# Kernel optimization log

Hardware: AMD Instinct MI355X
Metric: run time of the kernel (lower is better)

## Reference

```python
import jax, jax.numpy as jnp
import numpy as np

B, S, E, NUM_CLASSES = 4, 4096, 256, 16

def setup_inputs() -> dict:
    key = jax.random.key(0)
    ks = jax.random.split(key, 10)
    std = E ** -0.5
    return {
        "x":  jax.random.normal(ks[0], (B, S, E), dtype=jnp.float32),
        "wq": jax.random.normal(ks[1], (E, E), dtype=jnp.float32) * std,
        "bq": jnp.zeros((E,), dtype=jnp.float32),
        "wk": jax.random.normal(ks[2], (E, E), dtype=jnp.float32) * std,
        "bk": jnp.zeros((E,), dtype=jnp.float32),
        "wv": jax.random.normal(ks[3], (E, E), dtype=jnp.float32) * std,
        "bv": jnp.zeros((E,), dtype=jnp.float32),
        "wo": jax.random.normal(ks[4], (NUM_CLASSES, E), dtype=jnp.float32) * std,
        "bo": jnp.zeros((NUM_CLASSES,), dtype=jnp.float32),
    }

def reference(x, wq, bq, wk, bk, wv, bv, wo, bo):
    embed_dim = wq.shape[0]
    scaling = embed_dim ** -0.5  # float(embed_dim) ** (-0.5)
    # torch Linear: y = x @ W.T + b
    Q = jnp.einsum('bse,oe->bso', x, wq) + bq
    K = jnp.einsum('bse,oe->bso', x, wk) + bk
    V = jnp.einsum('bse,oe->bso', x, wv) + bv
    # scores: [B, S, S]
    scores = jnp.einsum('bqe,bke->bqk', Q, K) * scaling
    # original code has `/ (embed_dim ^ 0.5)`; intended math is / sqrt(embed_dim)
    attn = jax.nn.softmax(scores, axis=-1) * scaling
    attn_out = jnp.einsum('bqk,bke->bqe', attn, V)
    return jnp.einsum('bqe,oe->bqo', attn_out, wo) + bo
```

## Files before the change

kernel.cpp:

```cpp
#include <hip/hip_runtime.h>
#include <hip/hip_bf16.h>


#define S_ 4096
#define E_ 256
#define B_ 4
#define NC_ 16
#define BS_ (B_ * S_)
#define NS_ 4

typedef __attribute__((ext_vector_type(8))) short bf16x8;
typedef __attribute__((ext_vector_type(4))) float f32x4;

__device__ __forceinline__ unsigned short bf16_rtne(float f) {
    unsigned int u = __float_as_uint(f);
    return (unsigned short)((u + 0x7FFFu + ((u >> 16) & 1u)) >> 16);
}
__device__ __forceinline__ bf16x8 pack8(f32x4 a, f32x4 b) {
    bf16x8 r;
#pragma unroll
    for (int i = 0; i < 4; i++) r[i] = (short)bf16_rtne(a[i]);
#pragma unroll
    for (int i = 0; i < 4; i++) r[4 + i] = (short)bf16_rtne(b[i]);
    return r;
}
__device__ __forceinline__ void gl_lds16(const void* g, void* lds) {
    __builtin_amdgcn_global_load_lds(
        (const __attribute__((address_space(1))) unsigned int*)g,
        (__attribute__((address_space(3))) unsigned int*)lds, 16, 0, 0);
}

__global__ __launch_bounds__(256) void qkv_gemm(
    const float* __restrict__ x, const float* __restrict__ wq,
    const float* __restrict__ wk, const float* __restrict__ wv,
    const float* __restrict__ bq, const float* __restrict__ bk,
    const float* __restrict__ bv, short* __restrict__ Qb,
    short* __restrict__ Kb, short* __restrict__ Vtc) {
    __shared__ bf16x8 xt[256];
    __shared__ bf16x8 wt[1024];
    __shared__ short epi[16896];

    int t = threadIdx.x;
    int sel = blockIdx.x, m0 = blockIdx.y * 64;
    int lane = t & 63, wid = t >> 6, quad = lane >> 4, idx = lane & 15;

    const float* w = (sel == 0) ? wq : (sel == 1) ? wk : wv;
    const float* bias = (sel == 0) ? bq : (sel == 1) ? bk : bv;

    const float* xsrc = x + (size_t)(m0 + (t >> 2)) * E_ + (t & 3) * 8;

    f32x4 zf = {0.f, 0.f, 0.f, 0.f};
    f32x4 acc[16];
#pragma unroll
    for (int i = 0; i < 16; i++) acc[i] = zf;

    for (int kc = 0; kc < E_; kc += 32) {
        f32x4 a0 = *(const f32x4*)(xsrc + kc);
        f32x4 a1 = *(const f32x4*)(xsrc + kc + 4);
        xt[t] = pack8(a0, a1);
#pragma unroll
        for (int i = 0; i < 4; i++) {
            int p = i * 256 + t;
            const float* ws = w + (size_t)(p >> 2) * E_ + (p & 3) * 8 + kc;
            f32x4 b0 = *(const f32x4*)ws;
            f32x4 b1 = *(const f32x4*)(ws + 4);
            wt[p] = pack8(b0, b1);
        }
        __syncthreads();
        bf16x8 af = xt[(wid * 16 + idx) * 4 + quad];
#pragma unroll
        for (int ct = 0; ct < 16; ct++)
            acc[ct] = __builtin_amdgcn_mfma_f32_16x16x32_bf16(
                af, wt[(ct * 16 + idx) * 4 + quad], acc[ct], 0, 0, 0);
        __syncthreads();
    }

    int qr = quad * 4;
    if (sel == 2) {
#pragma unroll
        for (int ct = 0; ct < 16; ct++) {
            int e = ct * 16 + idx;
            float bb = bias[e];
#pragma unroll
            for (int r = 0; r < 4; r++) {
                int mr = wid * 16 + qr + r;
                int ckg = mr >> 5, sin = mr & 31;
                int sp = ((sin & 15) << 1) | (sin >> 4);
                int pos = (sp >> 3) ^ ((e >> 1) & 3);
                epi[ckg * 8192 + e * 32 + pos * 8 + (sp & 7)] =
                    (short)bf16_rtne(acc[ct][r] + bb);
            }
        }
        __syncthreads();
        size_t base = ((size_t)((m0 >> 12) * 128 + ((m0 & (S_ - 1)) >> 5))) * 8192;
#pragma unroll
        for (int j = 0; j < 8; j++) {
            int unit = j * 256 + t;
            *(bf16x8*)(Vtc + base + (size_t)unit * 8) = *(const bf16x8*)&epi[unit * 8];
        }
    } else {
        float alpha = (sel == 0) ? 0.0625f : 1.0f;
#pragma unroll
        for (int ct = 0; ct < 16; ct++) {
            int n = ct * 16 + idx;
            float bb = bias[n];
#pragma unroll
            for (int r = 0; r < 4; r++) {
                int row = wid * 16 + qr + r;
                int col = (sel == 1) ? ((((n >> 3) ^ (row & 7)) << 3) | (n & 7)) : n;
                epi[row * 264 + col] = (short)bf16_rtne((acc[ct][r] + bb) * alpha);
            }
        }
        __syncthreads();
        short* out = (sel == 0) ? Qb : Kb;
#pragma unroll
        for (int j = 0; j < 8; j++) {
            int g = j * 256 + t;
            int row = g >> 5, seg = g & 31;
            *(bf16x8*)(out + (size_t)(m0 + row) * E_ + seg * 8) =
                *(const bf16x8*)&epi[row * 264 + seg * 8];
        }
    }
}

__global__ __launch_bounds__(256, 2) void flash_attn(
    const short* __restrict__ Qb, const short* __restrict__ Kb,
    const short* __restrict__ Vtc, short* __restrict__ Opart,
    float* __restrict__ lpart) {
    __shared__ __align__(16) short lds[36864];

    int t = threadIdx.x;
    int b = blockIdx.z, slice = blockIdx.y, q0 = blockIdx.x * 128;
    int key0 = slice * (S_ / NS_);
    const int nchunk = (S_ / NS_) / 32;
    int lane = t & 63, wv = t >> 6, quad = lane >> 4, idx = lane & 15;

    bf16x8 qf[2][8];
#pragma unroll
    for (int u = 0; u < 2; u++) {
        const short* qrow = Qb + (size_t)(b * S_ + q0 + u * 64 + wv * 16 + idx) * E_ + quad * 8;
#pragma unroll
        for (int c = 0; c < 8; c++) qf[u][c] = *(const bf16x8*)(qrow + c * 32);
    }

    f32x4 zf = {0.f, 0.f, 0.f, 0.f};
    f32x4 oacc[2][16];
#pragma unroll
    for (int u = 0; u < 2; u++)
#pragma unroll
        for (int i = 0; i < 16; i++) oacc[u][i] = zf;
    float ls[2][4] = {{0, 0, 0, 0}, {0, 0, 0, 0}};

    const short* kg = Kb + (size_t)(b * S_ + key0) * E_ + lane * 8;
    const short* vg = Vtc + ((size_t)(b * 128 + (key0 >> 5))) * 8192 + lane * 8;
    short* psw = lds + 32768 + wv * 1024;
    unsigned int* pswu = (unsigned int*)psw;
    int vsw = (quad ^ ((idx >> 1) & 3)) << 3;

#pragma unroll
    for (int j = 0; j < 4; j++) gl_lds16(kg + (wv * 4 + j) * 512, &lds[(wv * 4 + j) * 512]);
#pragma unroll
    for (int j = 0; j < 4; j++) gl_lds16(vg + (wv * 4 + j) * 512, &lds[16384 + (wv * 4 + j) * 512]);
#pragma unroll
    for (int j = 0; j < 4; j++) gl_lds16(kg + 8192 + (wv * 4 + j) * 512, &lds[8192 + (wv * 4 + j) * 512]);
    __syncthreads();

    {
        f32x4 s[4] = {zf, zf, zf, zf};
#pragma unroll
        for (int c = 0; c < 8; c++) {
            int p = (((c * 4 + quad) ^ (idx & 7)) << 3);
            bf16x8 k0 = *(const bf16x8*)&lds[idx * 256 + p];
            bf16x8 k1 = *(const bf16x8*)&lds[(16 + idx) * 256 + p];
            s[0] = __builtin_amdgcn_mfma_f32_16x16x32_bf16(qf[0][c], k0, s[0], 0, 0, 0);
            s[1] = __builtin_amdgcn_mfma_f32_16x16x32_bf16(qf[0][c], k1, s[1], 0, 0, 0);
            s[2] = __builtin_amdgcn_mfma_f32_16x16x32_bf16(qf[1][c], k0, s[2], 0, 0, 0);
            s[3] = __builtin_amdgcn_mfma_f32_16x16x32_bf16(qf[1][c], k1, s[3], 0, 0, 0);
        }
#pragma unroll
        for (int u = 0; u < 2; u++)
#pragma unroll
            for (int r = 0; r < 4; r++) {
                float p0 = __expf(s[u * 2][r]);
                float p1 = __expf(s[u * 2 + 1][r]);
                ls[u][r] += p0 + p1;
                pswu[u * 256 + (quad * 4 + r) * 16 + idx] =
                    (unsigned int)bf16_rtne(p0) | ((unsigned int)bf16_rtne(p1) << 16);
            }
    }

    for (int ck = 0; ck < nchunk - 1; ck++) {
        __syncthreads();
        if (ck + 2 < nchunk) {
            const short* ks = kg + (size_t)(ck + 2) * 8192;
            short* kd = lds + (ck & 1) * 8192;
#pragma unroll
            for (int j = 0; j < 4; j++) gl_lds16(ks + (wv * 4 + j) * 512, &kd[(wv * 4 + j) * 512]);
        }
        {
            const short* vs = vg + (size_t)(ck + 1) * 8192;
            short* vd = lds + 16384 + ((ck + 1) & 1) * 8192;
#pragma unroll
            for (int j = 0; j < 4; j++) gl_lds16(vs + (wv * 4 + j) * 512, &vd[(wv * 4 + j) * 512]);
        }
        const short* kc = lds + ((ck + 1) & 1) * 8192;
        f32x4 s[4] = {zf, zf, zf, zf};
#pragma unroll
        for (int c = 0; c < 8; c++) {
            int p = (((c * 4 + quad) ^ (idx & 7)) << 3);
            bf16x8 k0 = *(const bf16x8*)&kc[idx * 256 + p];
            bf16x8 k1 = *(const bf16x8*)&kc[(16 + idx) * 256 + p];
            s[0] = __builtin_amdgcn_mfma_f32_16x16x32_bf16(qf[0][c], k0, s[0], 0, 0, 0);
            s[1] = __builtin_amdgcn_mfma_f32_16x16x32_bf16(qf[0][c], k1, s[1], 0, 0, 0);
            s[2] = __builtin_amdgcn_mfma_f32_16x16x32_bf16(qf[1][c], k0, s[2], 0, 0, 0);
            s[3] = __builtin_amdgcn_mfma_f32_16x16x32_bf16(qf[1][c], k1, s[3], 0, 0, 0);
        }
        bf16x8 af0 = *(const bf16x8*)&psw[idx * 32 + quad * 8];
        bf16x8 af1 = *(const bf16x8*)&psw[512 + idx * 32 + quad * 8];
#pragma unroll
        for (int u = 0; u < 2; u++)
#pragma unroll
            for (int r = 0; r < 4; r++) {
                float p0 = __expf(s[u * 2][r]);
                float p1 = __expf(s[u * 2 + 1][r]);
                ls[u][r] += p0 + p1;
                pswu[u * 256 + (quad * 4 + r) * 16 + idx] =
                    (unsigned int)bf16_rtne(p0) | ((unsigned int)bf16_rtne(p1) << 16);
            }
        const short* vc = lds + 16384 + (ck & 1) * 8192;
#pragma unroll
        for (int ct = 0; ct < 16; ct++) {
            bf16x8 v = *(const bf16x8*)&vc[(ct * 16 + idx) * 32 + vsw];
            oacc[0][ct] = __builtin_amdgcn_mfma_f32_16x16x32_bf16(af0, v, oacc[0][ct], 0, 0, 0);
            oacc[1][ct] = __builtin_amdgcn_mfma_f32_16x16x32_bf16(af1, v, oacc[1][ct], 0, 0, 0);
        }
    }
    __syncthreads();
    {
        bf16x8 af0 = *(const bf16x8*)&psw[idx * 32 + quad * 8];
        bf16x8 af1 = *(const bf16x8*)&psw[512 + idx * 32 + quad * 8];
        const short* vc = lds + 16384 + ((nchunk - 1) & 1) * 8192;
#pragma unroll
        for (int ct = 0; ct < 16; ct++) {
            bf16x8 v = *(const bf16x8*)&vc[(ct * 16 + idx) * 32 + vsw];
            oacc[0][ct] = __builtin_amdgcn_mfma_f32_16x16x32_bf16(af0, v, oacc[0][ct], 0, 0, 0);
            oacc[1][ct] = __builtin_amdgcn_mfma_f32_16x16x32_bf16(af1, v, oacc[1][ct], 0, 0, 0);
        }
    }
    __syncthreads();

#pragma unroll
    for (int u = 0; u < 2; u++)
#pragma unroll
        for (int r = 0; r < 4; r++) {
            float v = ls[u][r];
            v += __shfl_xor(v, 1);
            v += __shfl_xor(v, 2);
            v += __shfl_xor(v, 4);
            v += __shfl_xor(v, 8);
            if (idx == 0)
                lpart[(size_t)slice * BS_ + b * S_ + q0 + u * 64 + wv * 16 + quad * 4 + r] = v;
        }

    short* scr = lds + wv * 8192;
#pragma unroll
    for (int u = 0; u < 2; u++)
#pragma unroll
        for (int ct = 0; ct < 16; ct++) {
            int e = ct * 16 + idx;
#pragma unroll
            for (int r = 0; r < 4; r++) {
                int lr = quad * 4 + r;
                scr[u * 4096 + lr * 256 + ((((e >> 3) ^ (lr & 7)) << 3) | (e & 7))] =
                    (short)bf16_rtne(oacc[u][ct][r]);
            }
        }
#pragma unroll
    for (int u = 0; u < 2; u++) {
        size_t obase = ((size_t)slice * BS_ + (size_t)b * S_ + q0 + u * 64 + wv * 16) * E_;
#pragma unroll
        for (int j = 0; j < 8; j++) {
            int unit = j * 64 + lane;
            *(bf16x8*)(Opart + obase + (size_t)unit * 8) =
                *(const bf16x8*)&scr[u * 4096 + unit * 8];
        }
    }
}

__global__ __launch_bounds__(256) void proj_out(
    const short* __restrict__ Opart, const float* __restrict__ lpart,
    const float* __restrict__ wo, const float* __restrict__ bo,
    float* __restrict__ out) {
    __shared__ __align__(16) short at2[2][16384];
    int t = threadIdx.x;
    int m0 = blockIdx.x * 64;
    int lane = t & 63, wv = t >> 6, quad = lane >> 4, idx = lane & 15;

    bf16x8 bw[8];
#pragma unroll
    for (int c = 0; c < 8; c++) {
        const float* ws = wo + idx * E_ + c * 32 + quad * 8;
        f32x4 w0 = *(const f32x4*)ws;
        f32x4 w1 = *(const f32x4*)(ws + 4);
        bw[c] = pack8(w0, w1);
    }

#pragma unroll
    for (int j = 0; j < 8; j++)
        gl_lds16(Opart + (size_t)m0 * E_ + (wv * 8 + j) * 512 + lane * 8,
                 &at2[0][(wv * 8 + j) * 512]);

    f32x4 acc = {0.f, 0.f, 0.f, 0.f};
    for (int ns = 0; ns < NS_; ns++) {
        __syncthreads();
        if (ns + 1 < NS_) {
            const short* src = Opart + ((size_t)(ns + 1) * BS_ + m0) * E_ + lane * 8;
#pragma unroll
            for (int j = 0; j < 8; j++)
                gl_lds16(src + (wv * 8 + j) * 512, &at2[(ns + 1) & 1][(wv * 8 + j) * 512]);
        }
        const short* a = at2[ns & 1];
#pragma unroll
        for (int c = 0; c < 8; c++) {
            bf16x8 af = *(const bf16x8*)&a[(wv * 16 + idx) * 256 +
                                           ((((c * 4 + quad) ^ (idx & 7)) << 3))];
            acc = __builtin_amdgcn_mfma_f32_16x16x32_bf16(af, bw[c], acc, 0, 0, 0);
        }
    }
#pragma unroll
    for (int r = 0; r < 4; r++) {
        int m = m0 + wv * 16 + quad * 4 + r;
        float ltot = 0.f;
#pragma unroll
        for (int ns = 0; ns < NS_; ns++) ltot += lpart[(size_t)ns * BS_ + m];
        out[(size_t)m * NC_ + idx] = acc[r] * (0.0625f / ltot) + bo[idx];
    }
}

extern "C" void kernel_launch(void* const* d_in, const int* in_sizes, int n_in,
                              void* d_out, int out_size, void* d_ws, size_t ws_size,
                              hipStream_t stream) {
    const float* x  = (const float*)d_in[0];
    const float* wq = (const float*)d_in[1];
    const float* bq = (const float*)d_in[2];
    const float* wk = (const float*)d_in[3];
    const float* bk = (const float*)d_in[4];
    const float* wv = (const float*)d_in[5];
    const float* bv = (const float*)d_in[6];
    const float* wo = (const float*)d_in[7];
    const float* bo = (const float*)d_in[8];
    float* out = (float*)d_out;

    const size_t NEL = (size_t)BS_ * E_;
    short* Qb = (short*)d_ws;
    short* Kb = Qb + NEL;
    short* Vtc = Kb + NEL;
    short* Opart = Vtc + NEL;
    float* lpart = (float*)(Opart + (size_t)NS_ * NEL);

    qkv_gemm<<<dim3(3, BS_ / 64), 256, 0, stream>>>(x, wq, wk, wv, bq, bk, bv, Qb, Kb, Vtc);
    flash_attn<<<dim3(S_ / 128, NS_, B_), 256, 0, stream>>>(Qb, Kb, Vtc, Opart, lpart);
    proj_out<<<BS_ / 64, 256, 0, stream>>>(Opart, lpart, wo, bo, out);
}
```

Measured before the change: 178.9 us.

## Prepack x/W to bf16, double-buffer QKV GEMM loads, add MFMA priority and padding

Adds a pre-pass kernel that converts x and the three weight matrices to bf16 once, writing into the Opart workspace before it is used. The QKV GEMM then streams bf16 tiles into double-buffered swizzled LDS with direct global-to-LDS loads, removing the per-block fp32 conversion and one barrier per step. The attention kernel raises wave priority around MFMA blocks and pads the P scratch row stride to cut LDS bank conflicts. The cost is an extra launch and a full extra pass over x in memory.

```diff
diff --git a/kernel.cpp b/kernel.cpp
--- a/kernel.cpp
+++ b/kernel.cpp
@@ -29,50 +29,86 @@
         (const __attribute__((address_space(1))) unsigned int*)g,
         (__attribute__((address_space(3))) unsigned int*)lds, 16, 0, 0);
 }
-
-__global__ __launch_bounds__(256) void qkv_gemm(
+__device__ __forceinline__ int swz_u(int q) { return q ^ ((q >> 3) & 7); }
+
+#define XUNITS_ (BS_ * E_ / 8)
+#define WUNITS_ (3 * E_ * E_ / 8)
+__global__ __launch_bounds__(256) void pack_xw(
     const float* __restrict__ x, const float* __restrict__ wq,
     const float* __restrict__ wk, const float* __restrict__ wv,
+    short* __restrict__ xb, short* __restrict__ wb) {
+    int u = blockIdx.x * 256 + threadIdx.x;
+    const float* src;
+    short* dst;
+    if (u < XUNITS_) {
+        src = x + (size_t)u * 8;
+        dst = xb + (size_t)u * 8;
+    } else {
+        int u2 = u - XUNITS_;
+        int sel = u2 >> 13;
+        int off = (u2 & 8191) * 8;
+        src = ((sel == 0) ? wq : (sel == 1) ? wk : wv) + off;
+        dst = wb + sel * (E_ * E_) + off;
+    }
+    f32x4 a = *(const f32x4*)src;
+    f32x4 b = *(const f32x4*)(src + 4);
+    *(bf16x8*)dst = pack8(a, b);
+}
+
+__global__ __launch_bounds__(256) void qkv_gemm(
+    const short* __restrict__ xb, const short* __restrict__ wb,
     const float* __restrict__ bq, const float* __restrict__ bk,
     const float* __restrict__ bv, short* __restrict__ Qb,
     short* __restrict__ Kb, short* __restrict__ Vtc) {
-    __shared__ bf16x8 xt[256];
-    __shared__ bf16x8 wt[1024];
-    __shared__ short epi[16896];
+    __shared__ __align__(16) short stg[2][10240];
+    __shared__ __align__(16) short epi[16896];
 
     int t = threadIdx.x;
     int sel = blockIdx.x, m0 = blockIdx.y * 64;
     int lane = t & 63, wid = t >> 6, quad = lane >> 4, idx = lane & 15;
 
-    const float* w = (sel == 0) ? wq : (sel == 1) ? wk : wv;
+    const short* wsel = wb + sel * (E_ * E_);
     const float* bias = (sel == 0) ? bq : (sel == 1) ? bk : bv;
 
-    const float* xsrc = x + (size_t)(m0 + (t >> 2)) * E_ + (t & 3) * 8;
+    int ux = swz_u(t);
+    const short* xsrc = xb + (size_t)(m0 + (ux >> 2)) * E_ + (ux & 3) * 8;
+    const short* wsrc[4];
+#pragma unroll
+    for (int i = 0; i < 4; i++) {
+        int q = i * 256 + t, u = swz_u(q);
+        wsrc[i] = wsel + (size_t)(u >> 2) * E_ + (u & 3) * 8;
+    }
+
+    gl_lds16(xsrc, &stg[0][t * 8]);
+#pragma unroll
+    for (int i = 0; i < 4; i++) gl_lds16(wsrc[i], &stg[0][(256 + i * 256 + t) * 8]);
 
     f32x4 zf = {0.f, 0.f, 0.f, 0.f};
     f32x4 acc[16];
 #pragma unroll
     for (int i = 0; i < 16; i++) acc[i] = zf;
 
-    for (int kc = 0; kc < E_; kc += 32) {
-        f32x4 a0 = *(const f32x4*)(xsrc + kc);
-        f32x4 a1 = *(const f32x4*)(xsrc + kc + 4);
-        xt[t] = pack8(a0, a1);
-#pragma unroll
-        for (int i = 0; i < 4; i++) {
-            int p = i * 256 + t;
-            const float* ws = w + (size_t)(p >> 2) * E_ + (p & 3) * 8 + kc;
-            f32x4 b0 = *(const f32x4*)ws;
-            f32x4 b1 = *(const f32x4*)(ws + 4);
-            wt[p] = pack8(b0, b1);
-        }
+    int fo = (idx * 4 + quad) ^ (idx >> 1);
+
+    for (int it = 0; it < 8; it++) {
         __syncthreads();
-        bf16x8 af = xt[(wid * 16 + idx) * 4 + quad];
+        if (it < 7) {
+            int kc = (it + 1) * 32;
+            short* d = stg[(it + 1) & 1];
+            gl_lds16(xsrc + kc, &d[t * 8]);
+#pragma unroll
+            for (int i = 0; i < 4; i++)
+                gl_lds16(wsrc[i] + kc, &d[(256 + i * 256 + t) * 8]);
+        }
+        const short* cb = stg[it & 1];
+        bf16x8 af = *(const bf16x8*)&cb[(wid * 64 + fo) * 8];
+        const short* cw = &cb[(256 + fo) * 8];
+        __builtin_amdgcn_s_setprio(1);
 #pragma unroll
         for (int ct = 0; ct < 16; ct++)
             acc[ct] = __builtin_amdgcn_mfma_f32_16x16x32_bf16(
-                af, wt[(ct * 16 + idx) * 4 + quad], acc[ct], 0, 0, 0);
-        __syncthreads();
+                af, *(const bf16x8*)&cw[ct * 512], acc[ct], 0, 0, 0);
+        __builtin_amdgcn_s_setprio(0);
     }
 
     int qr = quad * 4;
@@ -127,7 +163,7 @@
     const short* __restrict__ Qb, const short* __restrict__ Kb,
     const short* __restrict__ Vtc, short* __restrict__ Opart,
     float* __restrict__ lpart) {
-    __shared__ __align__(16) short lds[36864];
+    __shared__ __align__(16) short lds[37888];
 
     int t = threadIdx.x;
     int b = blockIdx.z, slice = blockIdx.y, q0 = blockIdx.x * 128;
@@ -153,7 +189,7 @@
 
     const short* kg = Kb + (size_t)(b * S_ + key0) * E_ + lane * 8;
     const short* vg = Vtc + ((size_t)(b * 128 + (key0 >> 5))) * 8192 + lane * 8;
-    short* psw = lds + 32768 + wv * 1024;
+    short* psw = lds + 32768 + wv * 1280;
     unsigned int* pswu = (unsigned int*)psw;
     int vsw = (quad ^ ((idx >> 1) & 3)) << 3;
 
@@ -167,6 +203,7 @@
 
     {
         f32x4 s[4] = {zf, zf, zf, zf};
+        __builtin_amdgcn_s_setprio(1);
 #pragma unroll
         for (int c = 0; c < 8; c++) {
             int p = (((c * 4 + quad) ^ (idx & 7)) << 3);
@@ -177,6 +214,7 @@
             s[2] = __builtin_amdgcn_mfma_f32_16x16x32_bf16(qf[1][c], k0, s[2], 0, 0, 0);
             s[3] = __builtin_amdgcn_mfma_f32_16x16x32_bf16(qf[1][c], k1, s[3], 0, 0, 0);
         }
+        __builtin_amdgcn_s_setprio(0);
 #pragma unroll
         for (int u = 0; u < 2; u++)
 #pragma unroll
@@ -184,7 +222,7 @@
                 float p0 = __expf(s[u * 2][r]);
                 float p1 = __expf(s[u * 2 + 1][r]);
                 ls[u][r] += p0 + p1;
-                pswu[u * 256 + (quad * 4 + r) * 16 + idx] =
+                pswu[u * 320 + (quad * 4 + r) * 20 + idx] =
                     (unsigned int)bf16_rtne(p0) | ((unsigned int)bf16_rtne(p1) << 16);
             }
     }
@@ -205,6 +243,7 @@
         }
         const short* kc = lds + ((ck + 1) & 1) * 8192;
         f32x4 s[4] = {zf, zf, zf, zf};
+        __builtin_amdgcn_s_setprio(1);
 #pragma unroll
         for (int c = 0; c < 8; c++) {
             int p = (((c * 4 + quad) ^ (idx & 7)) << 3);
@@ -215,8 +254,9 @@
             s[2] = __builtin_amdgcn_mfma_f32_16x16x32_bf16(qf[1][c], k0, s[2], 0, 0, 0);
             s[3] = __builtin_amdgcn_mfma_f32_16x16x32_bf16(qf[1][c], k1, s[3], 0, 0, 0);
         }
-        bf16x8 af0 = *(const bf16x8*)&psw[idx * 32 + quad * 8];
-        bf16x8 af1 = *(const bf16x8*)&psw[512 + idx * 32 + quad * 8];
+        __builtin_amdgcn_s_setprio(0);
+        bf16x8 af0 = *(const bf16x8*)&psw[idx * 40 + quad * 8];
+        bf16x8 af1 = *(const bf16x8*)&psw[640 + idx * 40 + quad * 8];
 #pragma unroll
         for (int u = 0; u < 2; u++)
 #pragma unroll
@@ -224,28 +264,32 @@
                 float p0 = __expf(s[u * 2][r]);
                 float p1 = __expf(s[u * 2 + 1][r]);
                 ls[u][r] += p0 + p1;
-                pswu[u * 256 + (quad * 4 + r) * 16 + idx] =
+                pswu[u * 320 + (quad * 4 + r) * 20 + idx] =
                     (unsigned int)bf16_rtne(p0) | ((unsigned int)bf16_rtne(p1) << 16);
             }
         const short* vc = lds + 16384 + (ck & 1) * 8192;
+        __builtin_amdgcn_s_setprio(1);
 #pragma unroll
         for (int ct = 0; ct < 16; ct++) {
             bf16x8 v = *(const bf16x8*)&vc[(ct * 16 + idx) * 32 + vsw];
             oacc[0][ct] = __builtin_amdgcn_mfma_f32_16x16x32_bf16(af0, v, oacc[0][ct], 0, 0, 0);
             oacc[1][ct] = __builtin_amdgcn_mfma_f32_16x16x32_bf16(af1, v, oacc[1][ct], 0, 0, 0);
         }
+        __builtin_amdgcn_s_setprio(0);
     }
     __syncthreads();
     {
-        bf16x8 af0 = *(const bf16x8*)&psw[idx * 32 + quad * 8];
-        bf16x8 af1 = *(const bf16x8*)&psw[512 + idx * 32 + quad * 8];
+        bf16x8 af0 = *(const bf16x8*)&psw[idx * 40 + quad * 8];
+        bf16x8 af1 = *(const bf16x8*)&psw[640 + idx * 40 + quad * 8];
         const short* vc = lds + 16384 + ((nchunk - 1) & 1) * 8192;
+        __builtin_amdgcn_s_setprio(1);
 #pragma unroll
         for (int ct = 0; ct < 16; ct++) {
             bf16x8 v = *(const bf16x8*)&vc[(ct * 16 + idx) * 32 + vsw];
             oacc[0][ct] = __builtin_amdgcn_mfma_f32_16x16x32_bf16(af0, v, oacc[0][ct], 0, 0, 0);
             oacc[1][ct] = __builtin_amdgcn_mfma_f32_16x16x32_bf16(af1, v, oacc[1][ct], 0, 0, 0);
         }
+        __builtin_amdgcn_s_setprio(0);
     }
     __syncthreads();
 
@@ -357,8 +401,11 @@
     short* Vtc = Kb + NEL;
     short* Opart = Vtc + NEL;
     float* lpart = (float*)(Opart + (size_t)NS_ * NEL);
-
-    qkv_gemm<<<dim3(3, BS_ / 64), 256, 0, stream>>>(x, wq, wk, wv, bq, bk, bv, Qb, Kb, Vtc);
+    short* xb = Opart;
+    short* wb = Opart + NEL;
+
+    pack_xw<<<(XUNITS_ + WUNITS_) / 256, 256, 0, stream>>>(x, wq, wk, wv, xb, wb);
+    qkv_gemm<<<dim3(3, BS_ / 64), 256, 0, stream>>>(xb, wb, bq, bk, bv, Qb, Kb, Vtc);
     flash_attn<<<dim3(S_ / 128, NS_, B_), 256, 0, stream>>>(Qb, Kb, Vtc, Opart, lpart);
     proj_out<<<BS_ / 64, 256, 0, stream>>>(Opart, lpart, wo, bo, out);
 }
```

After: 179.8 us. About the same (+0.5%).
